# Optimization experiments

Measured on AMD Instinct MI355X. Metric: run time of the kernel, lower is better.

Reference implementation:

```python
import jax, jax.numpy as jnp
import numpy as np

H, T, D = 16, 4096, 64
N_SEQ = 8  # packed sequences -> cu_seqlens has N_SEQ+1 entries


def setup_inputs() -> dict:
    key = jax.random.key(0)
    kq, kk, kv, kc = jax.random.split(key, 4)
    q = jax.random.normal(kq, (1, H, T, D), dtype=jnp.float32)
    k = jax.random.normal(kk, (1, H, T, D), dtype=jnp.float32)
    v = jax.random.normal(kv, (1, H, T, D), dtype=jnp.float32)
    # cu_seqlens: monotonically increasing offsets, starts at 0, ends at T
    interior = jnp.sort(jax.random.randint(kc, (N_SEQ - 1,), 1, T, dtype=jnp.int32))
    cu_seqlens = jnp.concatenate([
        jnp.zeros((1,), jnp.int32), interior, jnp.full((1,), T, jnp.int32)
    ])
    return {"q": q, "k": k, "v": v, "cu_seqlens": cu_seqlens}


def reference(q, k, v, cu_seqlens):
    # Faithful to flash_attn_varlen_func(..., causal=False) on packed sequences:
    # non-causal attention restricted block-diagonally to each segment.
    scale = 1.0 / jnp.sqrt(jnp.asarray(D, q.dtype))
    # segment id for every token position
    pos = jnp.arange(T)
    seg = jnp.searchsorted(cu_seqlens[1:], pos, side="right")  # [T]
    mask = seg[:, None] == seg[None, :]                         # [T, T] block-diagonal
    # scores: [1, H, T, T]
    scores = jnp.einsum("bhqd,bhkd->bhqk", q, k) * scale
    neg = jnp.asarray(jnp.finfo(scores.dtype).min, scores.dtype)
    scores = jnp.where(mask[None, None], scores, neg)
    attn = jax.nn.softmax(scores, axis=-1)
    out = jnp.einsum("bhqk,bhkd->bhqd", attn, v)  # [1, H, T, D]
    return out
```

## Files before the change

kernel.cpp:

```cpp
#include <hip/hip_runtime.h>

#define HH 16
#define TT 4096
#define DD 64

typedef __attribute__((ext_vector_type(4))) _Float16 half4;
typedef __attribute__((ext_vector_type(4))) float float4v;

__global__ __launch_bounds__(256, 4) void pa_fwd(
    const float* __restrict__ qg, const float* __restrict__ kg,
    const float* __restrict__ vg, const int* __restrict__ cu,
    float* __restrict__ outg)
{
    __shared__ __align__(16) _Float16 Kl[2][64 * 64];
    __shared__ __align__(16) _Float16 Vl[2][64 * 64];

    const int tid  = threadIdx.x;
    const int lane = tid & 63;
    const int wave = tid >> 6;
    const int lr   = lane & 15;
    const int lg   = lane >> 4;

    const int bswz = ((int)blockIdx.x & 7) * 128 + ((int)blockIdx.x >> 3);
    const int h    = bswz >> 6;
    const int qblk = (bswz & 63) << 6;
    const int q    = qblk + wave * 16 + lr;

    int s = 0;
    while (cu[s + 1] <= q) ++s;
    const int lo = cu[s], hi = cu[s + 1];

    int sb = 0;
    while (cu[sb + 1] <= qblk) ++sb;
    const int blo = cu[sb];
    while (cu[sb + 1] <= qblk + 63) ++sb;
    const int bhi = cu[sb + 1];

    const int wlo = __shfl(lo, 0);
    const int whi = __shfl(hi, 15);
    const int mlo = __shfl(lo, 15);
    const int mhi = __shfl(hi, 0);

    const float* qrow = qg + ((size_t)h * TT + q) * DD;
    half4 qf[4];
#pragma unroll
    for (int ds = 0; ds < 4; ++ds) {
        float4v t4 = *(const float4v*)(qrow + ds * 16 + lg * 4);
#pragma unroll
        for (int j = 0; j < 4; ++j) qf[ds][j] = (_Float16)(t4[j] * 0.125f);
    }

    const float* kh_ = kg + (size_t)h * TT * DD;
    const float* vh_ = vg + (size_t)h * TT * DD;

    const int srow = tid >> 2;
    const int sch  = (tid & 3) << 4;
    const int vd   = tid & 63;

    unsigned kwr[4], vwr[4];
#pragma unroll
    for (int i = 0; i < 4; ++i) {
        const int ko8 = (tid & 3) * 4 + i;
        kwr[i] = (unsigned)(srow * 128 + 16 * ((ko8 >> 1) ^ (srow & 7)) +
                            8 * ((ko8 & 1) ^ ((srow >> 3) & 1)));
        const int vo8 = wave * 4 + i;
        vwr[i] = (unsigned)(vd * 128 + 16 * ((vo8 >> 1) ^ (vd & 7)) +
                            8 * ((vo8 & 1) ^ ((vd >> 3) & 1)));
    }
    unsigned rbase[4];
#pragma unroll
    for (int i = 0; i < 4; ++i)
        rbase[i] = (unsigned)(lr * 128 + 16 * (((2 * i + (lg >> 1))) ^ (lr & 7)) +
                              8 * ((lg & 1) ^ ((lr >> 3) & 1)));

    float4v kq[4];
    float vv[16];

    const int t0k = blo & ~63;
#define ISSUE(KT)                                                              \
    {                                                                          \
        int krow = (KT) + srow; if (krow > TT - 1) krow = TT - 1;              \
        const float4v* kp = (const float4v*)(kh_ + (size_t)krow * DD + sch);   \
        kq[0] = kp[0]; kq[1] = kp[1]; kq[2] = kp[2]; kq[3] = kp[3];            \
        _Pragma("unroll")                                                      \
        for (int c = 0; c < 16; ++c) {                                         \
            int vrow = (KT) + wave * 16 + c; if (vrow > TT - 1) vrow = TT - 1; \
            vv[c] = vh_[(size_t)vrow * DD + vd];                               \
        }                                                                      \
    }

    ISSUE(t0k);

    float4v acc[4];
#pragma unroll
    for (int dt = 0; dt < 4; ++dt) acc[dt] = (float4v){0.f, 0.f, 0.f, 0.f};
    float m_run = -1e30f, lsum = 0.f;

    int cur = 0;
    for (int kt = t0k; kt < bhi; kt += 64) {
        {
            char* Kb = (char*)Kl[cur];
            char* Vb = (char*)Vl[cur];
#pragma unroll
            for (int i = 0; i < 4; ++i) {
                half4 hk;
#pragma unroll
                for (int m = 0; m < 4; ++m) hk[m] = (_Float16)kq[i][m];
                *(half4*)(Kb + kwr[i]) = hk;
            }
#pragma unroll
            for (int i = 0; i < 4; ++i) {
                half4 hv;
#pragma unroll
                for (int m = 0; m < 4; ++m) hv[m] = (_Float16)vv[4 * i + m];
                *(half4*)(Vb + vwr[i]) = hv;
            }
        }
        __syncthreads();

        if (kt + 64 < bhi) ISSUE(kt + 64);

        if (!(kt + 64 <= wlo || kt >= whi)) {
            const char* Kb = (const char*)Kl[cur];
            const char* Vb = (const char*)Vl[cur];

            float st[4][4];
            const bool fullv = (kt >= mlo) && (kt + 64 <= mhi);
            __builtin_amdgcn_s_setprio(1);
#pragma unroll
            for (int t = 0; t < 4; ++t) {
                float4v sa = (float4v){0.f, 0.f, 0.f, 0.f};
#pragma unroll
                for (int ds = 0; ds < 4; ++ds) {
                    half4 kf = *(const half4*)(Kb + rbase[ds] + t * 2048);
                    sa = __builtin_amdgcn_mfma_f32_16x16x16f16(kf, qf[ds], sa, 0, 0, 0);
                }
                if (fullv) {
#pragma unroll
                    for (int j = 0; j < 4; ++j) st[t][j] = sa[j];
                } else {
#pragma unroll
                    for (int j = 0; j < 4; ++j) {
                        const int key = kt + t * 16 + lg * 4 + j;
                        st[t][j] = (key >= lo && key < hi) ? sa[j] : -1e30f;
                    }
                }
            }
            __builtin_amdgcn_s_setprio(0);

            float tx = -1e30f;
#pragma unroll
            for (int t = 0; t < 4; ++t)
#pragma unroll
                for (int j = 0; j < 4; ++j) tx = fmaxf(tx, st[t][j]);
            tx = fmaxf(tx, __shfl_xor(tx, 16));
            tx = fmaxf(tx, __shfl_xor(tx, 32));

            if (__any(tx > m_run + 8.f)) {
                const float mn = fmaxf(m_run, tx);
                const float a  = __expf(m_run - mn);
                lsum *= a;
#pragma unroll
                for (int dt = 0; dt < 4; ++dt)
#pragma unroll
                    for (int j = 0; j < 4; ++j) acc[dt][j] *= a;
                m_run = mn;
            }

            half4 pb[4];
            float ps = 0.f;
#pragma unroll
            for (int t = 0; t < 4; ++t)
#pragma unroll
                for (int j = 0; j < 4; ++j) {
                    const float e = __expf(st[t][j] - m_run);
                    ps += e;
                    pb[t][j] = (_Float16)e;
                }
            ps += __shfl_xor(ps, 16);
            ps += __shfl_xor(ps, 32);
            lsum += ps;

            __builtin_amdgcn_s_setprio(1);
#pragma unroll
            for (int t = 0; t < 4; ++t)
#pragma unroll
                for (int dt = 0; dt < 4; ++dt) {
                    half4 vf = *(const half4*)(Vb + rbase[t] + dt * 2048);
                    acc[dt] = __builtin_amdgcn_mfma_f32_16x16x16f16(vf, pb[t], acc[dt], 0, 0, 0);
                }
            __builtin_amdgcn_s_setprio(0);
        }
        cur ^= 1;
    }

    const float inv = 1.0f / lsum;
    float* orow = outg + ((size_t)h * TT + q) * DD;
#pragma unroll
    for (int dt = 0; dt < 4; ++dt) {
        float4v o;
#pragma unroll
        for (int j = 0; j < 4; ++j) o[j] = acc[dt][j] * inv;
        *(float4v*)(orow + dt * 16 + lg * 4) = o;
    }
#undef ISSUE
}

extern "C" void kernel_launch(void* const* d_in, const int* in_sizes, int n_in,
                              void* d_out, int out_size, void* d_ws, size_t ws_size,
                              hipStream_t stream) {
    const float* q  = (const float*)d_in[0];
    const float* k  = (const float*)d_in[1];
    const float* v  = (const float*)d_in[2];
    const int*   cu = (const int*)d_in[3];
    float* out = (float*)d_out;

    dim3 grid(HH * (TT / 64));
    dim3 block(256);
    hipLaunchKernelGGL(pa_fwd, grid, block, 0, stream, q, k, v, cu, out);
}
```

Baseline: 91.10 us.

## Split key tiles across wave pairs with 32-row query blocks and merge partial softmax

Each block now covers 32 query rows instead of 64, and the grid doubles. Two wave pairs handle alternating 64-key tiles of the same rows. Their partial accumulators, running max and sum are combined through shared memory at the end with a log-sum-exp merge. This raises block count and parallelism for a grid that is small relative to the GPU. In exchange, K/V tiles are loaded per block twice as often in total, and each wave does compute on only half the tiles while still taking part in every staging barrier.

```diff
diff --git a/kernel.cpp b/kernel.cpp
--- a/kernel.cpp
+++ b/kernel.cpp
@@ -20,20 +20,22 @@
     const int wave = tid >> 6;
     const int lr   = lane & 15;
     const int lg   = lane >> 4;
-
-    const int bswz = ((int)blockIdx.x & 7) * 128 + ((int)blockIdx.x >> 3);
-    const int h    = bswz >> 6;
-    const int qblk = (bswz & 63) << 6;
-    const int q    = qblk + wave * 16 + lr;
+    const int rsub = wave & 1;
+    const int par  = wave >> 1;
+
+    const int bswz = ((int)blockIdx.x & 7) * 256 + ((int)blockIdx.x >> 3);
+    const int h    = bswz >> 7;
+    const int qb0  = (bswz & 127) << 5;
+    const int q    = qb0 + rsub * 16 + lr;
 
     int s = 0;
     while (cu[s + 1] <= q) ++s;
     const int lo = cu[s], hi = cu[s + 1];
 
     int sb = 0;
-    while (cu[sb + 1] <= qblk) ++sb;
+    while (cu[sb + 1] <= qb0) ++sb;
     const int blo = cu[sb];
-    while (cu[sb + 1] <= qblk + 63) ++sb;
+    while (cu[sb + 1] <= qb0 + 31) ++sb;
     const int bhi = cu[sb + 1];
 
     const int wlo = __shfl(lo, 0);
@@ -120,7 +122,7 @@
 
         if (kt + 64 < bhi) ISSUE(kt + 64);
 
-        if (!(kt + 64 <= wlo || kt >= whi)) {
+        if ((((kt >> 6) & 1) == par) && !(kt + 64 <= wlo || kt >= whi)) {
             const char* Kb = (const char*)Kl[cur];
             const char* Vb = (const char*)Vl[cur];
 
@@ -194,14 +196,38 @@
         cur ^= 1;
     }
 
-    const float inv = 1.0f / lsum;
-    float* orow = outg + ((size_t)h * TT + q) * DD;
-#pragma unroll
-    for (int dt = 0; dt < 4; ++dt) {
-        float4v o;
-#pragma unroll
-        for (int j = 0; j < 4; ++j) o[j] = acc[dt][j] * inv;
-        *(float4v*)(orow + dt * 16 + lg * 4) = o;
+    float* mb = (float*)(&Kl[0][0]);
+    float* ml = (float*)(&Vl[0][0]);
+
+    __syncthreads();
+    if (wave >= 2) {
+#pragma unroll
+        for (int dt = 0; dt < 4; ++dt)
+            *(float4v*)(mb + (rsub * 16 + lr) * 64 + dt * 16 + lg * 4) = acc[dt];
+        if (lg == 0) {
+            ml[rsub * 16 + lr]      = m_run;
+            ml[32 + rsub * 16 + lr] = lsum;
+        }
+    }
+    __syncthreads();
+    if (wave < 2) {
+        const float mB = ml[rsub * 16 + lr];
+        const float lB = ml[32 + rsub * 16 + lr];
+        const float M  = fmaxf(m_run, mB);
+        const float eA = __expf(m_run - M);
+        const float eB = __expf(mB - M);
+        const float inv = 1.0f / (eA * lsum + eB * lB);
+
+        float* orow = outg + ((size_t)h * TT + q) * DD;
+#pragma unroll
+        for (int dt = 0; dt < 4; ++dt) {
+            float4v aB = *(const float4v*)(mb + (rsub * 16 + lr) * 64 + dt * 16 + lg * 4);
+            float4v o;
+#pragma unroll
+            for (int j = 0; j < 4; ++j)
+                o[j] = (eA * acc[dt][j] + eB * aB[j]) * inv;
+            *(float4v*)(orow + dt * 16 + lg * 4) = o;
+        }
     }
 #undef ISSUE
 }
@@ -215,7 +241,7 @@
     const int*   cu = (const int*)d_in[3];
     float* out = (float*)d_out;
 
-    dim3 grid(HH * (TT / 64));
+    dim3 grid(HH * (TT / 32));
     dim3 block(256);
     hipLaunchKernelGGL(pa_fwd, grid, block, 0, stream, q, k, v, cu, out);
 }
```

After: 126.1 us. +38.4%, slower.

## Prefetch two K/V tiles ahead, use exp2 softmax and packed fp16 converts

Applied to the files above, without the earlier changes.

Global loads of K and V now go into two register sets, so the tile two steps ahead is fetched while the current one is packed and consumed. This deepens the load pipeline. Log2(e) is folded into the Q scale so the softmax uses exp2 directly, and the rescale threshold is adjusted to match. fp32 to fp16 conversions now use the packed round-toward-zero instruction. The extra register set raises VGPR pressure and may hurt occupancy. The row clamping is dropped, which is safe only because the key tile range stays within T.

```diff
diff --git a/kernel.cpp b/kernel.cpp
--- a/kernel.cpp
+++ b/kernel.cpp
@@ -4,6 +4,7 @@
 #define TT 4096
 #define DD 64
 
+typedef __attribute__((ext_vector_type(2))) __fp16 half2r;
 typedef __attribute__((ext_vector_type(4))) _Float16 half4;
 typedef __attribute__((ext_vector_type(4))) float float4v;
 
@@ -41,13 +42,16 @@
     const int mlo = __shfl(lo, 15);
     const int mhi = __shfl(hi, 0);
 
+    const float qscale = 0.125f * 1.44269504088896f;
     const float* qrow = qg + ((size_t)h * TT + q) * DD;
     half4 qf[4];
 #pragma unroll
     for (int ds = 0; ds < 4; ++ds) {
         float4v t4 = *(const float4v*)(qrow + ds * 16 + lg * 4);
-#pragma unroll
-        for (int j = 0; j < 4; ++j) qf[ds][j] = (_Float16)(t4[j] * 0.125f);
+        half2r a = __builtin_amdgcn_cvt_pkrtz(t4[0] * qscale, t4[1] * qscale);
+        half2r b = __builtin_amdgcn_cvt_pkrtz(t4[2] * qscale, t4[3] * qscale);
+        qf[ds][0] = (_Float16)a[0]; qf[ds][1] = (_Float16)a[1];
+        qf[ds][2] = (_Float16)b[0]; qf[ds][3] = (_Float16)b[1];
     }
 
     const float* kh_ = kg + (size_t)h * TT * DD;
@@ -73,23 +77,45 @@
         rbase[i] = (unsigned)(lr * 128 + 16 * (((2 * i + (lg >> 1))) ^ (lr & 7)) +
                               8 * ((lg & 1) ^ ((lr >> 3) & 1)));
 
-    float4v kq[4];
-    float vv[16];
+    float4v kqA[4], kqB[4];
+    float vvA[16], vvB[16];
+
+#define ISSUE(KT, kq, vv)                                                      \
+    {                                                                          \
+        const float4v* kp = (const float4v*)(kh_ + (size_t)((KT) + srow) * DD + sch); \
+        kq[0] = kp[0]; kq[1] = kp[1]; kq[2] = kp[2]; kq[3] = kp[3];            \
+        const float* vp = vh_ + (size_t)((KT) + wave * 16) * DD + vd;          \
+        _Pragma("unroll")                                                      \
+        for (int c = 0; c < 16; ++c) vv[c] = vp[c * DD];                       \
+    }
+
+#define PACK(kq, vv, CUR)                                                      \
+    {                                                                          \
+        char* Kb = (char*)Kl[CUR];                                             \
+        char* Vb = (char*)Vl[CUR];                                             \
+        _Pragma("unroll")                                                      \
+        for (int i = 0; i < 4; ++i) {                                          \
+            half2r a = __builtin_amdgcn_cvt_pkrtz(kq[i][0], kq[i][1]);         \
+            half2r b = __builtin_amdgcn_cvt_pkrtz(kq[i][2], kq[i][3]);         \
+            half4 hk;                                                          \
+            hk[0] = (_Float16)a[0]; hk[1] = (_Float16)a[1];                    \
+            hk[2] = (_Float16)b[0]; hk[3] = (_Float16)b[1];                    \
+            *(half4*)(Kb + kwr[i]) = hk;                                       \
+        }                                                                      \
+        _Pragma("unroll")                                                      \
+        for (int i = 0; i < 4; ++i) {                                          \
+            half2r a = __builtin_amdgcn_cvt_pkrtz(vv[4 * i], vv[4 * i + 1]);   \
+            half2r b = __builtin_amdgcn_cvt_pkrtz(vv[4 * i + 2], vv[4 * i + 3]); \
+            half4 hv;                                                          \
+            hv[0] = (_Float16)a[0]; hv[1] = (_Float16)a[1];                    \
+            hv[2] = (_Float16)b[0]; hv[3] = (_Float16)b[1];                    \
+            *(half4*)(Vb + vwr[i]) = hv;                                       \
+        }                                                                      \
+    }
 
     const int t0k = blo & ~63;
-#define ISSUE(KT)                                                              \
-    {                                                                          \
-        int krow = (KT) + srow; if (krow > TT - 1) krow = TT - 1;              \
-        const float4v* kp = (const float4v*)(kh_ + (size_t)krow * DD + sch);   \
-        kq[0] = kp[0]; kq[1] = kp[1]; kq[2] = kp[2]; kq[3] = kp[3];            \
-        _Pragma("unroll")                                                      \
-        for (int c = 0; c < 16; ++c) {                                         \
-            int vrow = (KT) + wave * 16 + c; if (vrow > TT - 1) vrow = TT - 1; \
-            vv[c] = vh_[(size_t)vrow * DD + vd];                               \
-        }                                                                      \
-    }
-
-    ISSUE(t0k);
+    ISSUE(t0k, kqA, vvA);
+    if (t0k + 64 < bhi) ISSUE(t0k + 64, kqB, vvB);
 
     float4v acc[4];
 #pragma unroll
@@ -98,27 +124,12 @@
 
     int cur = 0;
     for (int kt = t0k; kt < bhi; kt += 64) {
-        {
-            char* Kb = (char*)Kl[cur];
-            char* Vb = (char*)Vl[cur];
-#pragma unroll
-            for (int i = 0; i < 4; ++i) {
-                half4 hk;
-#pragma unroll
-                for (int m = 0; m < 4; ++m) hk[m] = (_Float16)kq[i][m];
-                *(half4*)(Kb + kwr[i]) = hk;
-            }
-#pragma unroll
-            for (int i = 0; i < 4; ++i) {
-                half4 hv;
-#pragma unroll
-                for (int m = 0; m < 4; ++m) hv[m] = (_Float16)vv[4 * i + m];
-                *(half4*)(Vb + vwr[i]) = hv;
-            }
+        if (cur == 0) { PACK(kqA, vvA, 0); } else { PACK(kqB, vvB, 1); }
+        __syncthreads();
+        if (kt + 128 < bhi) {
+            if (cur == 0) { ISSUE(kt + 128, kqA, vvA); }
+            else          { ISSUE(kt + 128, kqB, vvB); }
         }
-        __syncthreads();
-
-        if (kt + 64 < bhi) ISSUE(kt + 64);
 
         if (!(kt + 64 <= wlo || kt >= whi)) {
             const char* Kb = (const char*)Kl[cur];
@@ -156,9 +167,9 @@
             tx = fmaxf(tx, __shfl_xor(tx, 16));
             tx = fmaxf(tx, __shfl_xor(tx, 32));
 
-            if (__any(tx > m_run + 8.f)) {
+            if (__any(tx > m_run + 11.54f)) {
                 const float mn = fmaxf(m_run, tx);
-                const float a  = __expf(m_run - mn);
+                const float a  = exp2f(m_run - mn);
                 lsum *= a;
 #pragma unroll
                 for (int dt = 0; dt < 4; ++dt)
@@ -170,13 +181,17 @@
             half4 pb[4];
             float ps = 0.f;
 #pragma unroll
-            for (int t = 0; t < 4; ++t)
-#pragma unroll
-                for (int j = 0; j < 4; ++j) {
-                    const float e = __expf(st[t][j] - m_run);
-                    ps += e;
-                    pb[t][j] = (_Float16)e;
-                }
+            for (int t = 0; t < 4; ++t) {
+                float e0 = exp2f(st[t][0] - m_run);
+                float e1 = exp2f(st[t][1] - m_run);
+                float e2 = exp2f(st[t][2] - m_run);
+                float e3 = exp2f(st[t][3] - m_run);
+                ps += (e0 + e1) + (e2 + e3);
+                half2r a = __builtin_amdgcn_cvt_pkrtz(e0, e1);
+                half2r b = __builtin_amdgcn_cvt_pkrtz(e2, e3);
+                pb[t][0] = (_Float16)a[0]; pb[t][1] = (_Float16)a[1];
+                pb[t][2] = (_Float16)b[0]; pb[t][3] = (_Float16)b[1];
+            }
             ps += __shfl_xor(ps, 16);
             ps += __shfl_xor(ps, 32);
             lsum += ps;
@@ -204,6 +219,7 @@
         *(float4v*)(orow + dt * 16 + lg * 4) = o;
     }
 #undef ISSUE
+#undef PACK
 }
 
 extern "C" void kernel_launch(void* const* d_in, const int* in_sizes, int n_in,
```

Result: slower. 186.6 us (+104.8%).
